# Kernel tuning notes

Measured on AMD Instinct MI355X. Metric: run time of the kernel, lower is better.

## Reference

```python
import jax, jax.numpy as jnp
import numpy as np

DEGREE = 10

def _chebyshev_basis(x, degree):
    # x: [B, F] -> basis: [B, F, degree+1] via T0=1, T1=t, Tk=2t*T_{k-1}-T_{k-2}
    t = jnp.tanh(x)
    polys = [jnp.ones_like(t), t]
    for _ in range(2, degree + 1):
        polys.append(2.0 * t * polys[-1] - polys[-2])
    return jnp.stack(polys, axis=-1)

def setup_inputs() -> dict:
    key = jax.random.key(0)
    k1, k2, k3, k4 = jax.random.split(key, 4)
    B, F_IN, F_OUT, D = 8192, 1024, 1024, DEGREE
    x = jax.random.normal(k1, (B, F_IN), dtype=jnp.float32)
    coeff_mean = jax.random.normal(k2, (F_IN, F_OUT, D + 1), dtype=jnp.float32) * 0.05
    coeff_log_var = jnp.full((F_IN, F_OUT, D + 1), -5.0, dtype=jnp.float32)
    base_weight = jax.random.normal(k3, (F_IN, F_OUT), dtype=jnp.float32) * 0.05
    # reparameterization noise, n_samples=1
    eps = jax.random.normal(k4, (1, F_IN, F_OUT, D + 1), dtype=jnp.float32)
    return {"x": x, "coeff_mean": coeff_mean, "coeff_log_var": coeff_log_var,
            "base_weight": base_weight, "eps": eps}

def reference(x, coeff_mean, coeff_log_var, base_weight, eps):
    basis = _chebyshev_basis(x, DEGREE)                      # [B, F_in, D+1]
    std = jnp.exp(0.5 * coeff_log_var)                       # [F_in, F_out, D+1]
    coeffs = coeff_mean[None] + eps * std[None]              # [S, F_in, F_out, D+1]
    poly_out = jnp.einsum('bin,sion->bo', basis, coeffs) / coeffs.shape[0]
    linear_out = x @ base_weight
    # KL with prior_mean=0, prior_var=1 (prior_scale=1.0)
    var = jnp.exp(coeff_log_var)
    kl = 0.5 * jnp.sum(var + coeff_mean ** 2 - 1.0 - coeff_log_var)
    return poly_out + linear_out, kl
```

## Files before the change

kernel.cpp:

```cpp
#include <hip/hip_runtime.h>

#define MDIM 8192
#define NDIM 1024
#define FIN  1024
#define DP1  11
#define KDIM 11264
#define KHALF 5632
#define ROWB 22528
#define HOFS 2883584u
#define NT 88
#define NITER 44

typedef __attribute__((ext_vector_type(8))) short short8;
typedef __attribute__((ext_vector_type(4))) float float4v;
typedef const __attribute__((address_space(1))) unsigned int* gptr_t;
typedef __attribute__((address_space(3))) unsigned int* lptr_t;

__device__ __forceinline__ unsigned int pk2(float a, float b) {
  unsigned int ua = __float_as_uint(a), ub = __float_as_uint(b);
  ua += 0x7FFFu + ((ua >> 16) & 1u);
  ub += 0x7FFFu + ((ub >> 16) & 1u);
  return __builtin_amdgcn_perm(ub, ua, 0x07060302);
}

__device__ __forceinline__ float fast_tanh(float x) {
  float e = __expf(2.f * x);
  return 1.f - 2.f / (e + 1.f);
}

struct Cheb { float t, T2, T3, T4, T5, T6, T7, T8, T9, T10; };
__device__ __forceinline__ Cheb cheb_eval(float x) {
  Cheb c;
  c.t = fast_tanh(x);
  const float t2 = 2.f * c.t;
  c.T2 = t2 * c.t - 1.f;
  c.T3 = t2 * c.T2 - c.t;
  c.T4 = t2 * c.T3 - c.T2;
  c.T5 = t2 * c.T4 - c.T3;
  c.T6 = t2 * c.T5 - c.T4;
  c.T7 = t2 * c.T6 - c.T5;
  c.T8 = t2 * c.T7 - c.T6;
  c.T9 = t2 * c.T8 - c.T7;
  c.T10 = t2 * c.T9 - c.T8;
  return c;
}

__device__ __forceinline__ void pack_pair(float xa, float xb, unsigned int* w) {
  Cheb a = cheb_eval(xa), b = cheb_eval(xb);
  w[0] = pk2(a.t, a.T2);  w[1] = pk2(a.T3, a.T4); w[2] = pk2(a.T5, a.T6);
  w[3] = pk2(a.T7, a.T8); w[4] = pk2(a.T9, a.T10); w[5] = pk2(xa, b.t);
  w[6] = pk2(b.T2, b.T3); w[7] = pk2(b.T4, b.T5);  w[8] = pk2(b.T6, b.T7);
  w[9] = pk2(b.T8, b.T9); w[10] = pk2(b.T10, xb);
}

__global__ __launch_bounds__(256) void prep_A_kernel(const float* __restrict__ x,
                                                     unsigned int* __restrict__ A) {
  __shared__ unsigned int rowbuf[5632];
  const int row = blockIdx.x;
  const int tid = threadIdx.x;
  float4 xv = ((const float4*)(x + (size_t)row * FIN))[tid];
  unsigned int w[22];
  pack_pair(xv.x, xv.y, w);
  pack_pair(xv.z, xv.w, w + 11);
#pragma unroll
  for (int j = 0; j < 22; j++) rowbuf[tid * 22 + j] = w[j];
  __syncthreads();
  uint2* dst = (uint2*)((char*)A + (size_t)row * ROWB);
  const uint2* src = (const uint2*)rowbuf;
#pragma unroll
  for (int j = 0; j < 11; j++) dst[tid + j * 256] = src[tid + j * 256];
}

__global__ __launch_bounds__(256) void prep_B_kernel(const float4* __restrict__ mean4,
    const float4* __restrict__ lv4, const float* __restrict__ W,
    const float4* __restrict__ eps4, unsigned short* __restrict__ Bt,
    float* __restrict__ partial, float* __restrict__ bias) {
  __shared__ float cf[2816];
  __shared__ unsigned int pkb[5632];
  __shared__ float wsum[4];
  const int tid = threadIdx.x;
  const int g = blockIdx.x >> 3;
  const int po = blockIdx.x & 7;
  float klp = 0.f;
  float biasAcc = 0.f;
#pragma unroll 1
  for (int pr = 0; pr < 4; ++pr) {
#pragma unroll
    for (int f = 0; f < 2; ++f) {
      const int i = g * 8 + pr * 2 + f;
      const size_t b4 = (size_t)i * 2816 + po * 352;
#pragma unroll
      for (int qq = 0; qq < 2; ++qq) {
        const int idx = qq * 256 + tid;
        if (idx < 352) {
          float4 m = mean4[b4 + idx];
          float4 l = lv4[b4 + idx];
          float4 e = eps4[b4 + idx];
          float s0 = __expf(0.5f * l.x), s1 = __expf(0.5f * l.y);
          float s2 = __expf(0.5f * l.z), s3 = __expf(0.5f * l.w);
          float4 c;
          c.x = fmaf(e.x, s0, m.x); c.y = fmaf(e.y, s1, m.y);
          c.z = fmaf(e.z, s2, m.z); c.w = fmaf(e.w, s3, m.w);
          klp += (s0 * s0 + m.x * m.x - 1.f - l.x) + (s1 * s1 + m.y * m.y - 1.f - l.y)
               + (s2 * s2 + m.z * m.z - 1.f - l.z) + (s3 * s3 + m.w * m.w - 1.f - l.w);
          ((float4*)cf)[f * 352 + idx] = c;
        }
      }
    }
    __syncthreads();
    if (tid < 128) {
      const int o = tid;
      const float* ca = &cf[o * DP1];
      const float* cb = &cf[1408 + o * DP1];
      const float wa = W[(size_t)(g * 8 + pr * 2) * NDIM + po * 128 + o];
      const float wb = W[(size_t)(g * 8 + pr * 2 + 1) * NDIM + po * 128 + o];
      biasAcc += ca[0] + cb[0];
      unsigned int* dq = &pkb[o * 44 + pr * 11];
      dq[0] = pk2(ca[1], ca[2]); dq[1] = pk2(ca[3], ca[4]); dq[2] = pk2(ca[5], ca[6]);
      dq[3] = pk2(ca[7], ca[8]); dq[4] = pk2(ca[9], ca[10]); dq[5] = pk2(wa, cb[1]);
      dq[6] = pk2(cb[2], cb[3]); dq[7] = pk2(cb[4], cb[5]); dq[8] = pk2(cb[6], cb[7]);
      dq[9] = pk2(cb[8], cb[9]); dq[10] = pk2(cb[10], wb);
    }
    __syncthreads();
  }
#pragma unroll
  for (int it = 0; it < 6; ++it) {
    const int cc = it * 256 + tid;
    if (cc < 1408) {
      const int o = cc / 11, c = cc - o * 11;
      uint4 v = *(const uint4*)&pkb[o * 44 + c * 4];
      *(uint4*)((char*)Bt + (size_t)(po * 128 + o) * ROWB + g * 176 + c * 16) = v;
    }
  }
  if (tid < 128) atomicAdd(&bias[po * 128 + tid], biasAcc);
#pragma unroll
  for (int off = 32; off > 0; off >>= 1) klp += __shfl_down(klp, off, 64);
  if ((tid & 63) == 0) wsum[tid >> 6] = klp;
  __syncthreads();
  if (tid == 0) partial[blockIdx.x] = wsum[0] + wsum[1] + wsum[2] + wsum[3];
}

__global__ __launch_bounds__(256) void reduce_kl_kernel(const float* __restrict__ partial,
                                                        float* __restrict__ kl_out) {
  __shared__ float wsum[4];
  const int tid = threadIdx.x;
  float s = 0.f;
#pragma unroll
  for (int k = 0; k < 4; k++) s += partial[tid + k * 256];
#pragma unroll
  for (int off = 32; off > 0; off >>= 1) s += __shfl_down(s, off, 64);
  if ((tid & 63) == 0) wsum[tid >> 6] = s;
  __syncthreads();
  if (tid == 0) kl_out[0] = 0.5f * (wsum[0] + wsum[1] + wsum[2] + wsum[3]);
}

#define VMW(N) asm volatile("s_waitcnt vmcnt(" #N ")" ::: "memory")

#define STG_A(p, h, t) do {                                                               \
    __builtin_amdgcn_global_load_lds((gptr_t)(gA + baseA0 + (h) * HOFS + (unsigned)(t) * 128u), \
        (lptr_t)(ldsp + (p) * 65536 + (h) * 16384 + d0), 16, 0, 0);                       \
    __builtin_amdgcn_global_load_lds((gptr_t)(gA + baseA1 + (h) * HOFS + (unsigned)(t) * 128u), \
        (lptr_t)(ldsp + (p) * 65536 + (h) * 16384 + d1), 16, 0, 0);                       \
  } while (0)

#define STG_B(p, h, t) do {                                                               \
    __builtin_amdgcn_global_load_lds((gptr_t)(gB + baseB0 + (h) * HOFS + (unsigned)(t) * 128u), \
        (lptr_t)(ldsp + (p) * 65536 + 32768 + (h) * 16384 + d0), 16, 0, 0);               \
    __builtin_amdgcn_global_load_lds((gptr_t)(gB + baseB1 + (h) * HOFS + (unsigned)(t) * 128u), \
        (lptr_t)(ldsp + (p) * 65536 + 32768 + (h) * 16384 + d1), 16, 0, 0);               \
  } while (0)

#define PHASE(p, f, STG_STMT, WAIT_STMT) do {                                             \
    const char* ap_ = ldsp + (p) * 65536 + aBase + (f) * 4096;                            \
    short8 a00 = *(const short8*)(ap_ + offk0);                                           \
    short8 a01 = *(const short8*)(ap_ + offk1);                                           \
    short8 a10 = *(const short8*)(ap_ + 2048 + offk0);                                    \
    short8 a11 = *(const short8*)(ap_ + 2048 + offk1);                                    \
    if ((f) == 0) {                                                                       \
      const char* bp_ = ldsp + (p) * 65536 + bBase;                                       \
      bfr[0][0] = *(const short8*)(bp_ + offk0);        bfr[0][1] = *(const short8*)(bp_ + offk1); \
      bfr[1][0] = *(const short8*)(bp_ + 2048 + offk0); bfr[1][1] = *(const short8*)(bp_ + 2048 + offk1); \
      bfr[2][0] = *(const short8*)(bp_ + 4096 + offk0); bfr[2][1] = *(const short8*)(bp_ + 4096 + offk1); \
      bfr[3][0] = *(const short8*)(bp_ + 6144 + offk0); bfr[3][1] = *(const short8*)(bp_ + 6144 + offk1); \
    }                                                                                     \
    STG_STMT;                                                                             \
    __builtin_amdgcn_s_barrier();                                                         \
    __builtin_amdgcn_sched_barrier(0);                                                    \
    __builtin_amdgcn_s_setprio(1);                                                        \
    _Pragma("unroll")                                                                     \
    for (int n_ = 0; n_ < 4; ++n_) {                                                      \
      acc[2 * (f)][n_]     = __builtin_amdgcn_mfma_f32_16x16x32_bf16(a00, bfr[n_][0], acc[2 * (f)][n_], 0, 0, 0);     \
      acc[2 * (f)][n_]     = __builtin_amdgcn_mfma_f32_16x16x32_bf16(a01, bfr[n_][1], acc[2 * (f)][n_], 0, 0, 0);     \
      acc[2 * (f) + 1][n_] = __builtin_amdgcn_mfma_f32_16x16x32_bf16(a10, bfr[n_][0], acc[2 * (f) + 1][n_], 0, 0, 0); \
      acc[2 * (f) + 1][n_] = __builtin_amdgcn_mfma_f32_16x16x32_bf16(a11, bfr[n_][1], acc[2 * (f) + 1][n_], 0, 0, 0); \
    }                                                                                     \
    __builtin_amdgcn_s_setprio(0);                                                        \
    WAIT_STMT;                                                                            \
    __builtin_amdgcn_s_barrier();                                                         \
    __builtin_amdgcn_sched_barrier(0);                                                    \
  } while (0)

__global__ __launch_bounds__(512, 2) void gemm_kernel(const unsigned short* __restrict__ A,
    const unsigned short* __restrict__ Bt, const float* __restrict__ bias,
    float* __restrict__ C) {
  __shared__ char lds[131072];
  char* ldsp = (char*)lds;
  const int tid = threadIdx.x;
  const int lane = tid & 63;
  const int wid = tid >> 6;
  const int wr = wid >> 2;
  const int wc = wid & 3;
  const int q = lane >> 4;
  const int r = lane & 15;
  const int bid = blockIdx.x;
  const int nt_ = bid & 3;
  const int kh = (bid >> 2) & 1;
  const int mt = bid >> 3;
  const int gm0 = mt * 256;
  const int gn0 = nt_ * 256;
  const unsigned kbyte0 = (unsigned)kh * KHALF * 2;

  const char* gA = (const char*)A;
  const char* gB = (const char*)Bt;

  const int c0 = tid, c1 = tid + 512;
  const int sr0 = c0 >> 3, sr1 = c1 >> 3;
  const unsigned baseA0 = (unsigned)(gm0 + sr0) * ROWB + kbyte0 + (((c0 & 7) ^ (sr0 & 7)) << 4);
  const unsigned baseA1 = (unsigned)(gm0 + sr1) * ROWB + kbyte0 + (((c1 & 7) ^ (sr1 & 7)) << 4);
  const unsigned baseB0 = (unsigned)(gn0 + sr0) * ROWB + kbyte0 + (((c0 & 7) ^ (sr0 & 7)) << 4);
  const unsigned baseB1 = (unsigned)(gn0 + sr1) * ROWB + kbyte0 + (((c1 & 7) ^ (sr1 & 7)) << 4);
  const int d0 = tid * 16, d1 = d0 + 8192;

  const int s7 = r & 7;
  const int offk0 = ((q ^ s7) << 4);
  const int offk1 = (((q + 4) ^ s7) << 4);
  const int aBase = wr * 16384 + r * 128;
  const int bBase = 32768 + (wc >> 1) * 16384 + ((wc & 1) * 64 + r) * 128;

  float4v acc[8][4];
#pragma unroll
  for (int m = 0; m < 8; m++)
#pragma unroll
    for (int n = 0; n < 4; n++) acc[m][n] = (float4v){0.f, 0.f, 0.f, 0.f};
  short8 bfr[4][2];

  STG_B(0, 0, 0); STG_B(0, 1, 0); STG_A(0, 0, 0); STG_A(0, 1, 0);
  STG_B(1, 0, 1); STG_B(1, 1, 1);
  VMW(4);
  __builtin_amdgcn_s_barrier();
  __builtin_amdgcn_sched_barrier(0);

#pragma unroll 1
  for (int i = 0; i < NITER - 1; ++i) {
    const int t1 = 2 * i + 1, t2 = 2 * i + 2, t3 = 2 * i + 3;
    PHASE(0, 0, STG_A(1, 0, t1), ;);
    PHASE(0, 1, STG_A(1, 1, t1), ;);
    PHASE(0, 2, STG_B(0, 0, t2), ;);
    PHASE(0, 3, STG_B(0, 1, t2), VMW(4));
    PHASE(1, 0, STG_A(0, 0, t2), ;);
    PHASE(1, 1, STG_A(0, 1, t2), ;);
    PHASE(1, 2, STG_B(1, 0, t3), ;);
    PHASE(1, 3, STG_B(1, 1, t3), VMW(4));
  }
  PHASE(0, 0, STG_A(1, 0, NT - 1), ;);
  PHASE(0, 1, STG_A(1, 1, NT - 1), ;);
  PHASE(0, 2, ;, ;);
  PHASE(0, 3, ;, VMW(0));
  PHASE(1, 0, ;, ;);
  PHASE(1, 1, ;, ;);
  PHASE(1, 2, ;, ;);
  PHASE(1, 3, ;, ;);

  float bv[4] = {0.f, 0.f, 0.f, 0.f};
  if (kh == 0) {
    const float* bp = bias + gn0 + wc * 64 + r;
#pragma unroll
    for (int n = 0; n < 4; n++) bv[n] = bp[n * 16];
  }
  float* Cb = C + (size_t)(gm0 + wr * 128) * NDIM + (gn0 + wc * 64);
#pragma unroll
  for (int m = 0; m < 8; m++)
#pragma unroll
    for (int n = 0; n < 4; n++)
#pragma unroll
      for (int v = 0; v < 4; v++)
        atomicAdd(&Cb[(size_t)(m * 16 + q * 4 + v) * NDIM + (n * 16 + r)], acc[m][n][v] + bv[n]);
}

extern "C" void kernel_launch(void* const* d_in, const int* in_sizes, int n_in,
                              void* d_out, int out_size, void* d_ws, size_t ws_size,
                              hipStream_t stream) {
  const float* x    = (const float*)d_in[0];
  const float* mean = (const float*)d_in[1];
  const float* lv   = (const float*)d_in[2];
  const float* W    = (const float*)d_in[3];
  const float* eps  = (const float*)d_in[4];
  float* out = (float*)d_out;

  unsigned short* Abf = (unsigned short*)d_ws;
  unsigned short* Bt  = (unsigned short*)((char*)d_ws + (size_t)MDIM * ROWB);
  float* bias    = (float*)((char*)d_ws + (size_t)MDIM * ROWB + (size_t)NDIM * ROWB);
  float* partial = bias + NDIM;
  float* kl = out + (size_t)MDIM * NDIM;

  hipMemsetAsync(bias, 0, NDIM * sizeof(float), stream);
  prep_A_kernel<<<MDIM, 256, 0, stream>>>(x, (unsigned int*)Abf);
  prep_B_kernel<<<1024, 256, 0, stream>>>((const float4*)mean, (const float4*)lv, W,
                                          (const float4*)eps, Bt, partial, bias);
  reduce_kl_kernel<<<1, 256, 0, stream>>>(partial, kl);
  hipMemsetAsync(out, 0, (size_t)MDIM * NDIM * sizeof(float), stream);
  gemm_kernel<<<256, 512, 0, stream>>>(Abf, Bt, bias, out);
}
```

Baseline: 414.5 us.

## Merge GEMM phase barriers, remap A staging, fold KL reduce into atomics

Each GEMM phase now issues its stage load and vmcnt wait, then passes a single barrier before the MFMAs, instead of taking two barriers per phase. This removes half the workgroup barriers in the main loop. A-tile staging is remapped so each thread loads one 64-row slice per fragment group, and B's second load targets contiguous rows. The separate KL reduction kernel is replaced by per-block atomicAdd into the output, with the output memset moved before the prep kernels, which cuts one launch but makes the KL sum order nondeterministic.

After: 413.0 us. About the same (-0.4%).

```diff
diff --git a/kernel.cpp b/kernel.cpp
--- a/kernel.cpp
+++ b/kernel.cpp
@@ -8,6 +8,7 @@
 #define KHALF 5632
 #define ROWB 22528
 #define HOFS 2883584u
+#define FGOFS 1441792u
 #define NT 88
 #define NITER 44
 
@@ -74,7 +75,7 @@
 __global__ __launch_bounds__(256) void prep_B_kernel(const float4* __restrict__ mean4,
     const float4* __restrict__ lv4, const float* __restrict__ W,
     const float4* __restrict__ eps4, unsigned short* __restrict__ Bt,
-    float* __restrict__ partial, float* __restrict__ bias) {
+    float* __restrict__ kl_out, float* __restrict__ bias) {
   __shared__ float cf[2816];
   __shared__ unsigned int pkb[5632];
   __shared__ float wsum[4];
@@ -137,40 +138,26 @@
   for (int off = 32; off > 0; off >>= 1) klp += __shfl_down(klp, off, 64);
   if ((tid & 63) == 0) wsum[tid >> 6] = klp;
   __syncthreads();
-  if (tid == 0) partial[blockIdx.x] = wsum[0] + wsum[1] + wsum[2] + wsum[3];
-}
-
-__global__ __launch_bounds__(256) void reduce_kl_kernel(const float* __restrict__ partial,
-                                                        float* __restrict__ kl_out) {
-  __shared__ float wsum[4];
-  const int tid = threadIdx.x;
-  float s = 0.f;
-#pragma unroll
-  for (int k = 0; k < 4; k++) s += partial[tid + k * 256];
-#pragma unroll
-  for (int off = 32; off > 0; off >>= 1) s += __shfl_down(s, off, 64);
-  if ((tid & 63) == 0) wsum[tid >> 6] = s;
-  __syncthreads();
-  if (tid == 0) kl_out[0] = 0.5f * (wsum[0] + wsum[1] + wsum[2] + wsum[3]);
+  if (tid == 0) atomicAdd(kl_out, 0.5f * (wsum[0] + wsum[1] + wsum[2] + wsum[3]));
 }
 
 #define VMW(N) asm volatile("s_waitcnt vmcnt(" #N ")" ::: "memory")
 
-#define STG_A(p, h, t) do {                                                               \
-    __builtin_amdgcn_global_load_lds((gptr_t)(gA + baseA0 + (h) * HOFS + (unsigned)(t) * 128u), \
-        (lptr_t)(ldsp + (p) * 65536 + (h) * 16384 + d0), 16, 0, 0);                       \
-    __builtin_amdgcn_global_load_lds((gptr_t)(gA + baseA1 + (h) * HOFS + (unsigned)(t) * 128u), \
-        (lptr_t)(ldsp + (p) * 65536 + (h) * 16384 + d1), 16, 0, 0);                       \
+#define STG_A(p, fg, t) do {                                                              \
+    __builtin_amdgcn_global_load_lds((gptr_t)(gA + baseAlo + (fg) * FGOFS + (unsigned)(t) * 128u), \
+        (lptr_t)(ldsp + (p) * 65536 + (fg) * 8192 + dA), 16, 0, 0);                       \
+    __builtin_amdgcn_global_load_lds((gptr_t)(gA + baseAhi + (fg) * FGOFS + (unsigned)(t) * 128u), \
+        (lptr_t)(ldsp + (p) * 65536 + 16384 + (fg) * 8192 + dA), 16, 0, 0);               \
   } while (0)
 
 #define STG_B(p, h, t) do {                                                               \
     __builtin_amdgcn_global_load_lds((gptr_t)(gB + baseB0 + (h) * HOFS + (unsigned)(t) * 128u), \
-        (lptr_t)(ldsp + (p) * 65536 + 32768 + (h) * 16384 + d0), 16, 0, 0);               \
+        (lptr_t)(ldsp + (p) * 65536 + 32768 + (h) * 16384 + dA), 16, 0, 0);               \
     __builtin_amdgcn_global_load_lds((gptr_t)(gB + baseB1 + (h) * HOFS + (unsigned)(t) * 128u), \
-        (lptr_t)(ldsp + (p) * 65536 + 32768 + (h) * 16384 + d1), 16, 0, 0);               \
+        (lptr_t)(ldsp + (p) * 65536 + 32768 + (h) * 16384 + 8192 + dA), 16, 0, 0);        \
   } while (0)
 
-#define PHASE(p, f, STG_STMT, WAIT_STMT) do {                                             \
+#define PH(p, f, STG_STMT, WAIT_STMT) do {                                                \
     const char* ap_ = ldsp + (p) * 65536 + aBase + (f) * 4096;                            \
     short8 a00 = *(const short8*)(ap_ + offk0);                                           \
     short8 a01 = *(const short8*)(ap_ + offk1);                                           \
@@ -184,6 +171,8 @@
       bfr[3][0] = *(const short8*)(bp_ + 6144 + offk0); bfr[3][1] = *(const short8*)(bp_ + 6144 + offk1); \
     }                                                                                     \
     STG_STMT;                                                                             \
+    WAIT_STMT;                                                                            \
+    __builtin_amdgcn_sched_barrier(0);                                                    \
     __builtin_amdgcn_s_barrier();                                                         \
     __builtin_amdgcn_sched_barrier(0);                                                    \
     __builtin_amdgcn_s_setprio(1);                                                        \
@@ -195,9 +184,6 @@
       acc[2 * (f) + 1][n_] = __builtin_amdgcn_mfma_f32_16x16x32_bf16(a11, bfr[n_][1], acc[2 * (f) + 1][n_], 0, 0, 0); \
     }                                                                                     \
     __builtin_amdgcn_s_setprio(0);                                                        \
-    WAIT_STMT;                                                                            \
-    __builtin_amdgcn_s_barrier();                                                         \
-    __builtin_amdgcn_sched_barrier(0);                                                    \
   } while (0)
 
 __global__ __launch_bounds__(512, 2) void gemm_kernel(const unsigned short* __restrict__ A,
@@ -223,13 +209,13 @@
   const char* gA = (const char*)A;
   const char* gB = (const char*)Bt;
 
-  const int c0 = tid, c1 = tid + 512;
-  const int sr0 = c0 >> 3, sr1 = c1 >> 3;
-  const unsigned baseA0 = (unsigned)(gm0 + sr0) * ROWB + kbyte0 + (((c0 & 7) ^ (sr0 & 7)) << 4);
-  const unsigned baseA1 = (unsigned)(gm0 + sr1) * ROWB + kbyte0 + (((c1 & 7) ^ (sr1 & 7)) << 4);
-  const unsigned baseB0 = (unsigned)(gn0 + sr0) * ROWB + kbyte0 + (((c0 & 7) ^ (sr0 & 7)) << 4);
-  const unsigned baseB1 = (unsigned)(gn0 + sr1) * ROWB + kbyte0 + (((c1 & 7) ^ (sr1 & 7)) << 4);
-  const int d0 = tid * 16, d1 = d0 + 8192;
+  const int srow = tid >> 3;
+  const int scol = ((tid & 7) ^ (srow & 7)) << 4;
+  const unsigned baseAlo = (unsigned)(gm0 + srow) * ROWB + kbyte0 + scol;
+  const unsigned baseAhi = baseAlo + 128u * ROWB;
+  const unsigned baseB0  = (unsigned)(gn0 + srow) * ROWB + kbyte0 + scol;
+  const unsigned baseB1  = (unsigned)(gn0 + 64 + srow) * ROWB + kbyte0 + scol;
+  const int dA = tid * 16;
 
   const int s7 = r & 7;
   const int offk0 = ((q ^ s7) << 4);
@@ -244,32 +230,33 @@
     for (int n = 0; n < 4; n++) acc[m][n] = (float4v){0.f, 0.f, 0.f, 0.f};
   short8 bfr[4][2];
 
-  STG_B(0, 0, 0); STG_B(0, 1, 0); STG_A(0, 0, 0); STG_A(0, 1, 0);
+  STG_A(0, 0, 0); STG_A(0, 1, 0); STG_B(0, 0, 0); STG_B(0, 1, 0);
   STG_B(1, 0, 1); STG_B(1, 1, 1);
   VMW(4);
+  __builtin_amdgcn_sched_barrier(0);
   __builtin_amdgcn_s_barrier();
   __builtin_amdgcn_sched_barrier(0);
 
 #pragma unroll 1
   for (int i = 0; i < NITER - 1; ++i) {
     const int t1 = 2 * i + 1, t2 = 2 * i + 2, t3 = 2 * i + 3;
-    PHASE(0, 0, STG_A(1, 0, t1), ;);
-    PHASE(0, 1, STG_A(1, 1, t1), ;);
-    PHASE(0, 2, STG_B(0, 0, t2), ;);
-    PHASE(0, 3, STG_B(0, 1, t2), VMW(4));
-    PHASE(1, 0, STG_A(0, 0, t2), ;);
-    PHASE(1, 1, STG_A(0, 1, t2), ;);
-    PHASE(1, 2, STG_B(1, 0, t3), ;);
-    PHASE(1, 3, STG_B(1, 1, t3), VMW(4));
-  }
-  PHASE(0, 0, STG_A(1, 0, NT - 1), ;);
-  PHASE(0, 1, STG_A(1, 1, NT - 1), ;);
-  PHASE(0, 2, ;, ;);
-  PHASE(0, 3, ;, VMW(0));
-  PHASE(1, 0, ;, ;);
-  PHASE(1, 1, ;, ;);
-  PHASE(1, 2, ;, ;);
-  PHASE(1, 3, ;, ;);
+    PH(0, 0, STG_A(1, 0, t1), ;);
+    PH(0, 1, STG_A(1, 1, t1), ;);
+    PH(0, 2, STG_B(0, 0, t2), ;);
+    PH(0, 3, STG_B(0, 1, t2), VMW(4));
+    PH(1, 0, STG_A(0, 0, t2), ;);
+    PH(1, 1, STG_A(0, 1, t2), ;);
+    PH(1, 2, STG_B(1, 0, t3), ;);
+    PH(1, 3, STG_B(1, 1, t3), VMW(4));
+  }
+  PH(0, 0, STG_A(1, 0, NT - 1), ;);
+  PH(0, 1, STG_A(1, 1, NT - 1), ;);
+  PH(0, 2, ;, ;);
+  PH(0, 3, ;, VMW(0));
+  PH(1, 0, ;, ;);
+  PH(1, 1, ;, ;);
+  PH(1, 2, ;, ;);
+  PH(1, 3, ;, ;);
 
   float bv[4] = {0.f, 0.f, 0.f, 0.f};
   if (kh == 0) {
@@ -299,15 +286,13 @@
 
   unsigned short* Abf = (unsigned short*)d_ws;
   unsigned short* Bt  = (unsigned short*)((char*)d_ws + (size_t)MDIM * ROWB);
-  float* bias    = (float*)((char*)d_ws + (size_t)MDIM * ROWB + (size_t)NDIM * ROWB);
-  float* partial = bias + NDIM;
+  float* bias = (float*)((char*)d_ws + (size_t)MDIM * ROWB + (size_t)NDIM * ROWB);
   float* kl = out + (size_t)MDIM * NDIM;
 
+  hipMemsetAsync(out, 0, ((size_t)MDIM * NDIM + 1) * sizeof(float), stream);
   hipMemsetAsync(bias, 0, NDIM * sizeof(float), stream);
   prep_A_kernel<<<MDIM, 256, 0, stream>>>(x, (unsigned int*)Abf);
   prep_B_kernel<<<1024, 256, 0, stream>>>((const float4*)mean, (const float4*)lv, W,
-                                          (const float4*)eps, Bt, partial, bias);
-  reduce_kl_kernel<<<1, 256, 0, stream>>>(partial, kl);
-  hipMemsetAsync(out, 0, (size_t)MDIM * NDIM * sizeof(float), stream);
+                                          (const float4*)eps, Bt, kl, bias);
   gemm_kernel<<<256, 512, 0, stream>>>(Abf, Bt, bias, out);
 }
```
